# Kernel optimization log

Hardware: AMD Instinct MI355X
Metric: run time of the kernel (lower is better)

The kernel has to match this reference:

```python
import jax, jax.numpy as jnp
import numpy as np

NUM_TAGS = 5

def setup_inputs() -> dict:
    key = jax.random.key(0)
    ks = jax.random.split(key, 8)
    B, N, K, Q = 2, 5, 5, 4
    Ls, Lq, D = 128, 128, 768
    inp = {
        'support_token_embedding': jax.random.normal(ks[0], (B * N * K, Ls, D), jnp.float32),
        'query_token_embedding': jax.random.normal(ks[1], (B * N * Q, Lq, D), jnp.float32),
        'support_mask': jnp.ones((B * N * K, Ls), jnp.float32),
        'query_mask': jnp.ones((B * N * Q, Lq), jnp.float32),
        'support_entity_label': jax.random.normal(ks[2], (B * N * K, Ls, NUM_TAGS), jnp.float32),
        'proj_w': jax.random.normal(ks[3], (D, 4 * D), jnp.float32) * 0.02,
        'proj_b': jnp.zeros((D,), jnp.float32),
        'rel_w1': jax.random.normal(ks[4], (D, 4 * D), jnp.float32) * 0.02,
        'rel_b1': jnp.zeros((D,), jnp.float32),
        'rel_w2': jax.random.normal(ks[5], (1, D), jnp.float32) * 0.02,
        'rel_b2': jnp.zeros((1,), jnp.float32),
        'B': B, 'N': N, 'K': K, 'Q': Q,
    }
    return inp

def _fuse(m1, m2):
    return jnp.concatenate([m1, m2, jnp.abs(m1 - m2), m1 * m2], axis=-1)

def reference(support_token_embedding, query_token_embedding, support_mask, query_mask,
              support_entity_label, proj_w, proj_b, rel_w1, rel_b1, rel_w2, rel_b2,
              B, N, K, Q):
    D = support_token_embedding.shape[-1]
    Lq = query_token_embedding.shape[1]

    # ---- cal_bio: per-(sample,shot) tag prototypes, vectorized ----
    labels = jnp.argmax(support_entity_label, axis=-1)                 # [BNK, Ls]
    onehot = jax.nn.one_hot(labels, NUM_TAGS, dtype=jnp.float32)       # [BNK, Ls, T]
    # tag 0 ('O') is additionally gated by the support mask
    masks = jnp.concatenate([onehot[:, :, :1] * support_mask[:, :, None], onehot[:, :, 1:]], axis=2)
    sums = jnp.einsum('blt,bld->btd', masks, support_token_embedding)  # [BNK, T, D]
    cnt = jnp.sum(masks, axis=1)[:, :, None]                           # [BNK, T, 1]
    proto = jnp.where(cnt > 0, sums / jnp.maximum(cnt, 1.0), 0.0)      # [BNK, T, D]
    proto = proto.reshape(B * N, K, NUM_TAGS, D).mean(axis=1)          # mean over K shots
    proto = proto.reshape(B, N, NUM_TAGS, D)                           # support_BIO

    # ---- expand to all (query, class) pairs: batch = B*N*Q*N ----
    BQ = B * N * Q * N
    support = jnp.broadcast_to(proto[:, None], (B, N * Q, N, NUM_TAGS, D)).reshape(BQ, NUM_TAGS, D)
    query = jnp.broadcast_to(query_token_embedding.reshape(B, N * Q, 1, Lq, D),
                             (B, N * Q, N, Lq, D)).reshape(BQ, Lq, D)
    qmask = jnp.broadcast_to(query_mask.reshape(B, N * Q, 1, Lq),
                             (B, N * Q, N, Lq)).reshape(BQ, Lq, 1)
    smask = jnp.ones((BQ, NUM_TAGS, 1), jnp.float32)

    # ---- CoAttention with additive mask bias + post-softmax mask multiply ----
    att = jnp.einsum('bsd,bqd->bsq', support, query) + smask * jnp.swapaxes(qmask, 1, 2) * 100.0
    support_ = jnp.einsum('bsq,bqd->bsd', jax.nn.softmax(att, axis=2), query) * smask
    query_ = jnp.einsum('bqs,bsd->bqd', jax.nn.softmax(jnp.swapaxes(att, 1, 2), axis=2), support) * qmask

    # ---- fuse + proj + relu ----
    es = jax.nn.relu(_fuse(support, support_) @ proj_w.T + proj_b)     # [BQ, T, D]
    eq = jax.nn.relu(_fuse(query, query_) @ proj_w.T + proj_b)        # [BQ, Lq, D]

    # ---- local aggregation: masked max + mean pooling ----
    eq_agg = jnp.concatenate([jnp.max(eq, axis=1), jnp.sum(eq, axis=1) / jnp.sum(qmask, axis=1)], axis=1)
    es_agg = jnp.concatenate([jnp.max(es, axis=1), jnp.sum(es, axis=1) / jnp.sum(smask, axis=1)], axis=1)

    # ---- relation MLP ----
    cat_seq = jnp.concatenate([eq_agg, es_agg], axis=1)                # [BQ, 4D]
    h = jax.nn.relu(cat_seq @ rel_w1.T + rel_b1)
    logits = h @ rel_w2.T + rel_b2                                     # [BQ, 1]
    return logits.reshape(B * N * Q, N)
```

## Files before the change

### kernel.cpp

```cpp
#include <hip/hip_runtime.h>

typedef unsigned short u16;
typedef __attribute__((ext_vector_type(8))) short short8;
typedef __attribute__((ext_vector_type(4))) float f32x4;

#define B_   2
#define N_   5
#define K_   5
#define Q_   4
#define T_   5
#define D_   768
#define L_   128
#define BN_  (B_*N_)
#define BNK_ (B_*N_*K_)
#define BQ_  (B_*N_*Q_*N_)
#define K4_  (4*D_)
#define KFQ  1536
#define AROWS 144

#define QEMB_N  (40*128*768)
#define PROJW_N (768*3072)

__device__ __forceinline__ float bf2f(u16 u) {
    return __uint_as_float(((unsigned)u) << 16);
}
__device__ __forceinline__ u16 f2bf(float f) {
    unsigned u = __float_as_uint(f);
    return (u16)((u + 0x7fffu + ((u >> 16) & 1u)) >> 16);
}
__device__ __forceinline__ void gl_lds16(const u16* g, u16* l) {
    __builtin_amdgcn_global_load_lds(
        (const __attribute__((address_space(1))) unsigned int*)g,
        (__attribute__((address_space(3))) unsigned int*)l, 16, 0, 0);
}

__global__ void k_convert3(const float* __restrict__ q, const float* __restrict__ pw,
                           const float* __restrict__ rw, u16* __restrict__ qo,
                           u16* __restrict__ po, u16* __restrict__ ro) {
    const long n1 = QEMB_N / 4, n2 = PROJW_N / 4;
    const long total = n1 + 2 * n2;
    for (long i = (long)blockIdx.x * 256 + threadIdx.x; i < total; i += (long)gridDim.x * 256) {
        const float* src; u16* dst; long k;
        if (i < n1)            { src = q;  dst = qo; k = i; }
        else if (i < n1 + n2)  { src = pw; dst = po; k = i - n1; }
        else                   { src = rw; dst = ro; k = i - n1 - n2; }
        float4 v = ((const float4*)src)[k];
        u16 o[4] = {f2bf(v.x), f2bf(v.y), f2bf(v.z), f2bf(v.w)};
        *(uint2*)(dst + k * 4) = *(const uint2*)o;
    }
}

__global__ void k_proto_shot(const float* __restrict__ label, const float* __restrict__ smask,
                             const float* __restrict__ semb, float* __restrict__ proto_shot) {
    int bnk = blockIdx.x;
    int s = blockIdx.y;
    __shared__ int   s_tag[L_];
    __shared__ float s_w[L_];
    __shared__ float s_cnt[T_];
    int tid = threadIdx.x;
    if (tid < L_) {
        const float* lp = label + ((long)bnk * L_ + tid) * T_;
        float best = lp[0]; int bi = 0;
        #pragma unroll
        for (int t = 1; t < T_; ++t) { float v = lp[t]; if (v > best) { best = v; bi = t; } }
        s_tag[tid] = bi;
        s_w[tid]   = (bi == 0) ? smask[(long)bnk * L_ + tid] : 1.0f;
    }
    __syncthreads();
    if (tid < T_) {
        float c = 0.f;
        for (int l = 0; l < L_; ++l) if (s_tag[l] == tid) c += s_w[l];
        s_cnt[tid] = c;
    }
    __syncthreads();
    float acc[T_] = {};
    for (int l = 0; l < L_; ++l) {
        float w = s_w[l]; int tg = s_tag[l];
        float e = semb[((long)bnk * L_ + l) * D_ + tid + s * 256] * w;
        #pragma unroll
        for (int t = 0; t < T_; ++t) acc[t] += (tg == t) ? e : 0.0f;
    }
    int d = tid + s * 256;
    #pragma unroll
    for (int t = 0; t < T_; ++t) {
        float c = s_cnt[t];
        float v = (c > 0.f) ? acc[t] / fmaxf(c, 1.f) : 0.f;
        proto_shot[(bnk * T_ + t) * D_ + d] = v;
    }
}

__global__ void k_proto_mean(const float* __restrict__ proto_shot,
                             float* __restrict__ proto_f32, u16* __restrict__ proto_bf) {
    int idx = blockIdx.x * 256 + threadIdx.x;
    if (idx >= BN_ * T_ * D_) return;
    int bn = idx / (T_ * D_);
    int rem = idx - bn * (T_ * D_);
    float s = 0.f;
    #pragma unroll
    for (int k = 0; k < K_; ++k) s += proto_shot[(bn * K_ + k) * (T_ * D_) + rem];
    s *= (1.f / K_);
    proto_f32[idx] = s;
    proto_bf[idx]  = f2bf(s);
}

__global__ void k_attn(const float* __restrict__ qemb, const float* __restrict__ qmask_g,
                       const float* __restrict__ proto_f32,
                       u16* __restrict__ qf, u16* __restrict__ sup_ws,
                       float* __restrict__ p2m_ws, float* __restrict__ qssum_ws) {
    int x = blockIdx.x;
    int xcd = x & 7, slot = x >> 3;
    int g = (slot / 5) * 8 + xcd;
    int n2 = slot % 5;
    int bq = g * 5 + n2;
    int q_idx = g;
    int bn = (bq / (N_ * Q_ * N_)) * N_ + (bq % N_);
    __shared__ float s_proto[T_ * D_];
    __shared__ float s_att[T_][L_];
    __shared__ float s_ps[T_][L_];
    __shared__ float s_p2[L_][8];
    __shared__ float s_qm[L_];
    __shared__ float s_m2[L_][33];
    int tid = threadIdx.x;
    for (int i = tid; i < T_ * D_; i += 256) s_proto[i] = proto_f32[bn * T_ * D_ + i];
    if (tid < L_) s_qm[tid] = qmask_g[(long)q_idx * L_ + tid];
    __syncthreads();
    for (int p = tid; p < T_ * L_; p += 256) {
        int t = p >> 7, q = p & (L_ - 1);
        const float* pp = s_proto + t * D_;
        const float4* qp = (const float4*)(qemb + ((size_t)q_idx * L_ + q) * D_);
        float acc = 0.f;
        #pragma unroll 4
        for (int d = 0; d < D_ / 4; ++d) {
            float4 v = qp[d];
            acc += v.x * pp[4 * d] + v.y * pp[4 * d + 1] + v.z * pp[4 * d + 2] + v.w * pp[4 * d + 3];
        }
        s_att[t][q] = acc + 100.f * s_qm[q];
    }
    __syncthreads();
    if (tid < T_) {
        int t = tid; float m = -1e30f;
        for (int q = 0; q < L_; ++q) m = fmaxf(m, s_att[t][q]);
        float ss = 0.f;
        for (int q = 0; q < L_; ++q) { float e = __expf(s_att[t][q] - m); s_ps[t][q] = e; ss += e; }
        float inv = 1.f / ss;
        for (int q = 0; q < L_; ++q) s_ps[t][q] *= inv;
    } else if (tid >= 128) {
        int q = tid - 128; float m = -1e30f;
        float e[T_];
        #pragma unroll
        for (int t = 0; t < T_; ++t) m = fmaxf(m, s_att[t][q]);
        float ss = 0.f;
        #pragma unroll
        for (int t = 0; t < T_; ++t) { e[t] = __expf(s_att[t][q] - m); ss += e[t]; }
        float inv = s_qm[q] / ss;
        #pragma unroll
        for (int t = 0; t < T_; ++t) {
            s_p2[q][t] = e[t] * inv;
            p2m_ws[((size_t)bq * T_ + t) * L_ + q] = e[t] * inv;
        }
    } else if (tid == 5) {
        float s = 0.f;
        for (int q = 0; q < L_; ++q) s += s_qm[q];
        qssum_ws[bq] = s;
    }
    __syncthreads();
    u16* qfb = qf + (size_t)bq * AROWS * KFQ;
    {
        float acc[T_][3] = {};
        #pragma unroll 4
        for (int q = 0; q < L_; ++q) {
            const float* qp = qemb + ((size_t)q_idx * L_ + q) * D_;
            float qv[3];
            #pragma unroll
            for (int s = 0; s < 3; ++s) qv[s] = qp[tid + s * 256];
            #pragma unroll
            for (int t = 0; t < T_; ++t) {
                float p = s_ps[t][q];
                #pragma unroll
                for (int s = 0; s < 3; ++s) acc[t][s] += p * qv[s];
            }
        }
        #pragma unroll
        for (int t = 0; t < T_; ++t) {
            u16* er = qfb + (size_t)(128 + t) * KFQ;
            #pragma unroll
            for (int s = 0; s < 3; ++s) {
                int d = tid + s * 256;
                float p = s_proto[t * D_ + d];
                float sv = acc[t][s];
                sup_ws[((size_t)bq * T_ + t) * D_ + d] = f2bf(sv);
                er[d]       = f2bf(fabsf(p - sv));
                er[768 + d] = f2bf(p * sv);
            }
        }
    }
    {
        int row_b = tid & 127, half = tid >> 7;
        float pr[T_];
        #pragma unroll
        for (int t = 0; t < T_; ++t) pr[t] = s_p2[row_b][t];
        int d2 = tid & 31, r0 = tid >> 5;
        for (int slab = 0; slab < 24; ++slab) {
            #pragma unroll
            for (int j = 0; j < 16; ++j) {
                int col = half * 16 + j;
                int d = slab * 32 + col;
                float m2 = pr[0] * s_proto[d] + pr[1] * s_proto[D_ + d]
                         + pr[2] * s_proto[2 * D_ + d] + pr[3] * s_proto[3 * D_ + d]
                         + pr[4] * s_proto[4 * D_ + d];
                s_m2[row_b][col] = m2;
            }
            __syncthreads();
            #pragma unroll
            for (int k = 0; k < 16; ++k) {
                int row = r0 + k * 8;
                int dd = slab * 32 + d2;
                float m2 = s_m2[row][d2];
                float qv = qemb[((size_t)q_idx * L_ + row) * D_ + dd];
                u16* qr = qfb + (size_t)row * KFQ;
                qr[dd]        = f2bf(fabsf(qv - m2));
                qr[768 + dd]  = f2bf(qv * m2);
            }
            __syncthreads();
        }
    }
    {
        u16* pr2 = qfb + (size_t)133 * KFQ;
        short8 z = short8{0, 0, 0, 0, 0, 0, 0, 0};
        for (int i = tid; i < (11 * KFQ) / 8; i += 256) *(short8*)(pr2 + i * 8) = z;
    }
}

#define SWZ(g, r) (((g) << 4) + ((r) ^ ((g) << 2)))
__global__ __launch_bounds__(256) void k_gemm_g1(const u16* __restrict__ qemb_bf,
                                                 const u16* __restrict__ proto_bf,
                                                 const u16* __restrict__ projw_bf,
                                                 u16* __restrict__ g1) {
    int mbase = blockIdx.y * 128;
    int jbase = blockIdx.x * 128;
    __shared__ __align__(16) u16 sA[8 * 512];
    __shared__ __align__(16) u16 sB[8 * 512];
    int tid = threadIdx.x;
    int lane = tid & 63, w = tid >> 6, quad = lane >> 4, l16 = lane & 15;
    f32x4 zero = {0.f, 0.f, 0.f, 0.f};
    f32x4 acc[8][2];
    #pragma unroll
    for (int rt = 0; rt < 8; ++rt) { acc[rt][0] = zero; acc[rt][1] = zero; }

    for (int kt = 0; kt < 24; ++kt) {
        int k0 = kt * 32;
        __syncthreads();
        #pragma unroll
        for (int j = 0; j < 2; ++j) {
            int v = tid + j * 256, row = v >> 2, g = v & 3;
            *(uint4*)(sB + (((row >> 4) << 6) + SWZ(g, row & 15)) * 8) =
                *(const uint4*)(projw_bf + (size_t)(jbase + row) * K4_ + k0 + g * 8);
            int grow = mbase + row;
            uint4 av = uint4{0u, 0u, 0u, 0u};
            if (grow < 5120)      av = *(const uint4*)(qemb_bf + (size_t)grow * D_ + k0 + g * 8);
            else if (grow < 5170) av = *(const uint4*)(proto_bf + (size_t)(grow - 5120) * D_ + k0 + g * 8);
            *(uint4*)(sA + (((row >> 4) << 6) + SWZ(g, row & 15)) * 8) = av;
        }
        __syncthreads();
        short8 af[8], bfr[2];
        #pragma unroll
        for (int rt = 0; rt < 8; ++rt)
            af[rt] = *(const short8*)(sA + ((rt << 6) + SWZ(quad, l16)) * 8);
        #pragma unroll
        for (int jj = 0; jj < 2; ++jj)
            bfr[jj] = *(const short8*)(sB + (((w * 2 + jj) << 6) + SWZ(quad, l16)) * 8);
        #pragma unroll
        for (int rt = 0; rt < 8; ++rt)
            #pragma unroll
            for (int jj = 0; jj < 2; ++jj)
                acc[rt][jj] = __builtin_amdgcn_mfma_f32_16x16x32_bf16(af[rt], bfr[jj], acc[rt][jj], 0, 0, 0);
    }
    #pragma unroll
    for (int jj = 0; jj < 2; ++jj) {
        int col = jbase + (w * 2 + jj) * 16 + l16;
        #pragma unroll
        for (int rt = 0; rt < 8; ++rt)
            #pragma unroll
            for (int r = 0; r < 4; ++r) {
                int row = mbase + rt * 16 + quad * 4 + r;
                g1[(size_t)row * D_ + col] = f2bf(acc[rt][jj][r]);
            }
    }
}

__global__ __launch_bounds__(256) void k_gemm_w2(const u16* __restrict__ sup_ws,
                                                 const u16* __restrict__ proto_bf,
                                                 const u16* __restrict__ projw_bf,
                                                 u16* __restrict__ sw2, u16* __restrict__ pw2) {
    int mbase = blockIdx.y * 128;
    int jbase = blockIdx.x * 128;
    __shared__ __align__(16) u16 sA[8 * 512];
    __shared__ __align__(16) u16 sB[8 * 512];
    int tid = threadIdx.x;
    int lane = tid & 63, w = tid >> 6, quad = lane >> 4, l16 = lane & 15;
    f32x4 zero = {0.f, 0.f, 0.f, 0.f};
    f32x4 acc[8][2];
    #pragma unroll
    for (int rt = 0; rt < 8; ++rt) { acc[rt][0] = zero; acc[rt][1] = zero; }

    for (int kt = 0; kt < 24; ++kt) {
        int k0 = kt * 32;
        __syncthreads();
        #pragma unroll
        for (int j = 0; j < 2; ++j) {
            int v = tid + j * 256, row = v >> 2, g = v & 3;
            *(uint4*)(sB + (((row >> 4) << 6) + SWZ(g, row & 15)) * 8) =
                *(const uint4*)(projw_bf + (size_t)(jbase + row) * K4_ + 768 + k0 + g * 8);
            int grow = mbase + row;
            uint4 av = uint4{0u, 0u, 0u, 0u};
            if (grow < 1000)      av = *(const uint4*)(sup_ws + (size_t)grow * D_ + k0 + g * 8);
            else if (grow < 1050) av = *(const uint4*)(proto_bf + (size_t)(grow - 1000) * D_ + k0 + g * 8);
            *(uint4*)(sA + (((row >> 4) << 6) + SWZ(g, row & 15)) * 8) = av;
        }
        __syncthreads();
        short8 af[8], bfr[2];
        #pragma unroll
        for (int rt = 0; rt < 8; ++rt)
            af[rt] = *(const short8*)(sA + ((rt << 6) + SWZ(quad, l16)) * 8);
        #pragma unroll
        for (int jj = 0; jj < 2; ++jj)
            bfr[jj] = *(const short8*)(sB + (((w * 2 + jj) << 6) + SWZ(quad, l16)) * 8);
        #pragma unroll
        for (int rt = 0; rt < 8; ++rt)
            #pragma unroll
            for (int jj = 0; jj < 2; ++jj)
                acc[rt][jj] = __builtin_amdgcn_mfma_f32_16x16x32_bf16(af[rt], bfr[jj], acc[rt][jj], 0, 0, 0);
    }
    #pragma unroll
    for (int jj = 0; jj < 2; ++jj) {
        int col = jbase + (w * 2 + jj) * 16 + l16;
        #pragma unroll
        for (int rt = 0; rt < 8; ++rt)
            #pragma unroll
            for (int r = 0; r < 4; ++r) {
                int row = mbase + rt * 16 + quad * 4 + r;
                if (row < 1000)      sw2[(size_t)row * D_ + col] = f2bf(acc[rt][jj][r]);
                else if (row < 1050) pw2[(size_t)(row - 1000) * D_ + col] = f2bf(acc[rt][jj][r]);
            }
    }
}

__global__ __launch_bounds__(256, 3) void k_gemm_q(
        const u16* __restrict__ qf, const u16* __restrict__ projw_bf,
        const float* __restrict__ projb, const u16* __restrict__ g1,
        const u16* __restrict__ pw2, const u16* __restrict__ sw2,
        const float* __restrict__ p2m, const float* __restrict__ qssum_ws,
        u16* __restrict__ cat_ws) {
    int x = blockIdx.x;
    int xcd = x & 7, slot = x >> 3;
    int bq = (slot / 12) * 8 + xcd;
    int jbase = (slot % 12) * 64;
    int q_idx = bq / N_;
    int bn = (bq / (N_ * Q_ * N_)) * N_ + (bq % N_);
    __shared__ __align__(16) u16 sT[2][(AROWS + 64) * 32];
    __shared__ float s_p2mL[T_ * 128];
    __shared__ float s_pw2L[T_ * 64];
    int tid = threadIdx.x;
    int lane = tid & 63, w = tid >> 6, quad = lane >> 4, l16 = lane & 15;
    int srow = lane >> 2, sko = lane & 3;
    const u16* Ab = qf + ((size_t)bq * AROWS + srow) * KFQ + sko * 8;
    const u16* Bb = projw_bf + (size_t)(jbase + srow) * K4_ + 1536 + sko * 8;

    f32x4 zero = {0.f, 0.f, 0.f, 0.f};
    f32x4 acc[9];
    #pragma unroll
    for (int rt = 0; rt < 9; ++rt) acc[rt] = zero;

    auto issue = [&](int kt, int b) {
        int k0 = kt * 32;
        u16* base = sT[b];
        gl_lds16(Ab + (size_t)(w * 16) * KFQ + k0, base + (w * 16) * 32);
        gl_lds16(Ab + (size_t)(64 + w * 16) * KFQ + k0, base + (64 + w * 16) * 32);
        if (w == 0) gl_lds16(Ab + (size_t)128 * KFQ + k0, base + 128 * 32);
        gl_lds16(Bb + (size_t)(w * 16) * K4_ + k0, base + (AROWS + w * 16) * 32);
    };

    issue(0, 0);
    for (int kt = 0; kt < KFQ / 32; ++kt) {
        int cur = kt & 1;
        __syncthreads();
        if (kt + 1 < KFQ / 32) issue(kt + 1, 1 - cur);
        const u16* base = sT[cur];
        short8 af[9], bf1;
        #pragma unroll
        for (int rt = 0; rt < 9; ++rt)
            af[rt] = *(const short8*)(base + (rt * 16 + l16) * 32 + quad * 8);
        bf1 = *(const short8*)(base + (AROWS + w * 16 + l16) * 32 + quad * 8);
        #pragma unroll
        for (int rt = 0; rt < 9; ++rt)
            acc[rt] = __builtin_amdgcn_mfma_f32_16x16x32_bf16(af[rt], bf1, acc[rt], 0, 0, 0);
    }
    for (int i = tid; i < T_ * 128; i += 256) s_p2mL[i] = p2m[(size_t)bq * (T_ * 128) + i];
    for (int i = tid; i < T_ * 64; i += 256)
        s_pw2L[i] = bf2f(pw2[(size_t)(bn * T_ + (i >> 6)) * D_ + jbase + (i & 63)]);
    __syncthreads();
    float inv_qs = 1.f / qssum_ws[bq];
    {
        int c = w * 16 + l16;
        int col = jbase + c;
        float bias = projb[col];
        float qmax = 0.f, qsum = 0.f, smax = 0.f, ssum = 0.f;
        #pragma unroll
        for (int rt = 0; rt < 8; ++rt) {
            #pragma unroll
            for (int r = 0; r < 4; ++r) {
                int row = rt * 16 + quad * 4 + r;
                float g1v = bf2f(g1[(size_t)(q_idx * 128 + row) * D_ + col]);
                float mix = s_p2mL[row] * s_pw2L[c]
                          + s_p2mL[128 + row] * s_pw2L[64 + c]
                          + s_p2mL[256 + row] * s_pw2L[128 + c]
                          + s_p2mL[384 + row] * s_pw2L[192 + c]
                          + s_p2mL[512 + row] * s_pw2L[256 + c];
                float v = fmaxf(acc[rt][r] + g1v + mix + bias, 0.f);
                qmax = fmaxf(qmax, v); qsum += v;
            }
        }
        #pragma unroll
        for (int r = 0; r < 4; ++r) {
            int t = quad * 4 + r;
            if (t < T_) {
                float g1v = bf2f(g1[(size_t)(5120 + bn * T_ + t) * D_ + col]);
                float s2v = bf2f(sw2[(size_t)(bq * T_ + t) * D_ + col]);
                float v = fmaxf(acc[8][r] + g1v + s2v + bias, 0.f);
                smax = fmaxf(smax, v); ssum += v;
            }
        }
        qmax = fmaxf(qmax, __shfl_xor(qmax, 16, 64)); qmax = fmaxf(qmax, __shfl_xor(qmax, 32, 64));
        qsum += __shfl_xor(qsum, 16, 64);             qsum += __shfl_xor(qsum, 32, 64);
        smax = fmaxf(smax, __shfl_xor(smax, 16, 64)); smax = fmaxf(smax, __shfl_xor(smax, 32, 64));
        ssum += __shfl_xor(ssum, 16, 64);             ssum += __shfl_xor(ssum, 32, 64);
        if (quad == 0) {
            u16* cp = cat_ws + (size_t)bq * K4_;
            cp[col]           = f2bf(qmax);
            cp[D_ + col]      = f2bf(qsum * inv_qs);
            cp[2 * D_ + col]  = f2bf(smax);
            cp[3 * D_ + col]  = f2bf(ssum * 0.2f);
        }
    }
}

#define AST  40
__global__ __launch_bounds__(256) void k_relmlp(const u16* __restrict__ cat_ws,
                                                const u16* __restrict__ w1,
                                                float* __restrict__ part) {
    int mbase = blockIdx.y * 64;
    int jbase = blockIdx.x * 128;
    int ks = blockIdx.z;
    __shared__ __align__(16) u16 sA[64 * AST];
    __shared__ __align__(16) u16 sB[128 * AST];
    int tid = threadIdx.x;
    int lane = tid & 63, w = tid >> 6, quad = lane >> 4, l16 = lane & 15;
    f32x4 zero = {0.f, 0.f, 0.f, 0.f};
    f32x4 acc[4][2];
    #pragma unroll
    for (int rt = 0; rt < 4; ++rt) { acc[rt][0] = zero; acc[rt][1] = zero; }

    for (int kt = ks * 12; kt < ks * 12 + 12; ++kt) {
        int k0 = kt * 32;
        __syncthreads();
        {
            int row = tid >> 2, ko = (tid & 3) * 8;
            int grow = mbase + row;
            short8 val = short8{0, 0, 0, 0, 0, 0, 0, 0};
            if (grow < BQ_) val = *(const short8*)(cat_ws + (size_t)grow * K4_ + k0 + ko);
            *(short8*)(sA + row * AST + ko) = val;
        }
        for (int u = tid; u < 512; u += 256) {
            int row = u >> 2, ko = (u & 3) * 8;
            *(short8*)(sB + row * AST + ko) =
                *(const short8*)(w1 + (size_t)(jbase + row) * K4_ + k0 + ko);
        }
        __syncthreads();
        short8 af[4], bfr[2];
        #pragma unroll
        for (int rt = 0; rt < 4; ++rt)
            af[rt] = *(const short8*)(sA + (rt * 16 + l16) * AST + quad * 8);
        #pragma unroll
        for (int jj = 0; jj < 2; ++jj)
            bfr[jj] = *(const short8*)(sB + ((2 * w + jj) * 16 + l16) * AST + quad * 8);
        #pragma unroll
        for (int rt = 0; rt < 4; ++rt)
            #pragma unroll
            for (int jj = 0; jj < 2; ++jj)
                acc[rt][jj] = __builtin_amdgcn_mfma_f32_16x16x32_bf16(af[rt], bfr[jj], acc[rt][jj], 0, 0, 0);
    }
    #pragma unroll
    for (int jj = 0; jj < 2; ++jj) {
        int col = jbase + (2 * w + jj) * 16 + l16;
        #pragma unroll
        for (int rt = 0; rt < 4; ++rt) {
            #pragma unroll
            for (int r = 0; r < 4; ++r) {
                int grow = mbase + rt * 16 + quad * 4 + r;
                if (grow < BQ_)
                    part[((size_t)ks * BQ_ + grow) * D_ + col] = acc[rt][jj][r];
            }
        }
    }
}

__global__ void k_rel_fin(const float* __restrict__ part, const float* __restrict__ b1,
                          const float* __restrict__ w2, const float* __restrict__ b2,
                          float* __restrict__ out) {
    int bq = blockIdx.x, tid = threadIdx.x;
    float a = 0.f;
    #pragma unroll
    for (int s = 0; s < 3; ++s) {
        int col = tid + s * 256;
        float sum = 0.f;
        #pragma unroll
        for (int ks = 0; ks < 8; ++ks) sum += part[((size_t)ks * BQ_ + bq) * D_ + col];
        float h = fmaxf(sum + b1[col], 0.f);
        a += h * w2[col];
    }
    __shared__ float red[256];
    red[tid] = a; __syncthreads();
    for (int off = 128; off >= 1; off >>= 1) {
        if (tid < off) red[tid] += red[tid + off];
        __syncthreads();
    }
    if (tid == 0) out[bq] = red[0] + b2[0];
}

extern "C" void kernel_launch(void* const* d_in, const int* in_sizes, int n_in,
                              void* d_out, int out_size, void* d_ws, size_t ws_size,
                              hipStream_t stream) {
    (void)in_sizes; (void)n_in; (void)out_size; (void)ws_size;
    const float* semb  = (const float*)d_in[0];
    const float* qemb  = (const float*)d_in[1];
    const float* smask = (const float*)d_in[2];
    const float* qmask = (const float*)d_in[3];
    const float* label = (const float*)d_in[4];
    const float* projw = (const float*)d_in[5];
    const float* projb = (const float*)d_in[6];
    const float* relw1 = (const float*)d_in[7];
    const float* relb1 = (const float*)d_in[8];
    const float* relw2 = (const float*)d_in[9];
    const float* relb2 = (const float*)d_in[10];

    char* ws = (char*)d_ws;
    u16*   qemb_bf   = (u16*)  (ws + 0);
    u16*   projw_bf  = (u16*)  (ws + 7864320);
    u16*   relw1_bf  = (u16*)  (ws + 12582912);
    float* proto_shot= (float*)(ws + 17301504);
    float* proto_f32 = (float*)(ws + 18069504);
    u16*   proto_bf  = (u16*)  (ws + 18223104);
    float* qssum     = (float*)(ws + 18299904);
    u16*   sup_ws    = (u16*)  (ws + 18300800);
    float* p2m_ws    = (float*)(ws + 19836800);
    u16*   pw2_ws    = (u16*)  (ws + 20348800);
    u16*   sw2_ws    = (u16*)  (ws + 20425600);
    u16*   cat_ws    = (u16*)  (ws + 21961600);
    u16*   g1_ws     = (u16*)  (ws + 23190400);
    float* part_ws   = (float*)(ws + 31251328);
    u16*   qf_ws     = (u16*)  (ws + 36166528);

    k_convert3<<<2048, 256, 0, stream>>>(qemb, projw, relw1, qemb_bf, projw_bf, relw1_bf);
    k_proto_shot<<<dim3(BNK_, 3), 256, 0, stream>>>(label, smask, semb, proto_shot);
    k_proto_mean<<<150, 256, 0, stream>>>(proto_shot, proto_f32, proto_bf);
    k_attn<<<BQ_, 256, 0, stream>>>(qemb, qmask, proto_f32, qf_ws, sup_ws, p2m_ws, qssum);
    k_gemm_g1<<<dim3(6, 41), 256, 0, stream>>>(qemb_bf, proto_bf, projw_bf, g1_ws);
    k_gemm_w2<<<dim3(6, 9), 256, 0, stream>>>(sup_ws, proto_bf, projw_bf, sw2_ws, pw2_ws);
    k_gemm_q<<<2400, 256, 0, stream>>>(qf_ws, projw_bf, projb, g1_ws, pw2_ws, sw2_ws,
                                       p2m_ws, qssum, cat_ws);
    k_relmlp<<<dim3(6, 4, 8), 256, 0, stream>>>(cat_ws, relw1_bf, part_ws);
    k_rel_fin<<<BQ_, 256, 0, stream>>>(part_ws, relb1, relw2, relb2, (float*)d_out);
}
```

Measured before the change: 535.9 us.

## Widen k_gemm_q column tile to 128 and regroup blocks by query

Each k_gemm_q block now computes 128 output columns instead of 64, with each wave holding two B fragments and reusing every A fragment load across two MFMAs. This halves the grid and halves how many times the 144-row query-feature A tile is streamed from memory. The block-to-(bq, column) mapping is also reordered so consecutive slots on an XCD share the same bq group. In exchange the block needs more accumulator registers and more LDS, which may reduce occupancy under launch_bounds(256,3).

Measured after the change: 583.9 us. 1.09x slower.

```diff
diff --git a/kernel.cpp b/kernel.cpp
--- a/kernel.cpp
+++ b/kernel.cpp
@@ -353,13 +353,15 @@
         u16* __restrict__ cat_ws) {
     int x = blockIdx.x;
     int xcd = x & 7, slot = x >> 3;
-    int bq = (slot / 12) * 8 + xcd;
-    int jbase = (slot % 12) * 64;
+    int i = slot / 6, jslot = slot % 6;
+    int g = (i / 5) * 8 + xcd;
+    int bq = g * 5 + (i % 5);
+    int jbase = jslot * 128;
     int q_idx = bq / N_;
     int bn = (bq / (N_ * Q_ * N_)) * N_ + (bq % N_);
-    __shared__ __align__(16) u16 sT[2][(AROWS + 64) * 32];
+    __shared__ __align__(16) u16 sT[2][(AROWS + 128) * 32];
     __shared__ float s_p2mL[T_ * 128];
-    __shared__ float s_pw2L[T_ * 64];
+    __shared__ float s_pw2L[T_ * 128];
     int tid = threadIdx.x;
     int lane = tid & 63, w = tid >> 6, quad = lane >> 4, l16 = lane & 15;
     int srow = lane >> 2, sko = lane & 3;
@@ -367,9 +369,9 @@
     const u16* Bb = projw_bf + (size_t)(jbase + srow) * K4_ + 1536 + sko * 8;
 
     f32x4 zero = {0.f, 0.f, 0.f, 0.f};
-    f32x4 acc[9];
-    #pragma unroll
-    for (int rt = 0; rt < 9; ++rt) acc[rt] = zero;
+    f32x4 acc[9][2];
+    #pragma unroll
+    for (int rt = 0; rt < 9; ++rt) { acc[rt][0] = zero; acc[rt][1] = zero; }
 
     auto issue = [&](int kt, int b) {
         int k0 = kt * 32;
@@ -378,6 +380,7 @@
         gl_lds16(Ab + (size_t)(64 + w * 16) * KFQ + k0, base + (64 + w * 16) * 32);
         if (w == 0) gl_lds16(Ab + (size_t)128 * KFQ + k0, base + 128 * 32);
         gl_lds16(Bb + (size_t)(w * 16) * K4_ + k0, base + (AROWS + w * 16) * 32);
+        gl_lds16(Bb + (size_t)(64 + w * 16) * K4_ + k0, base + (AROWS + 64 + w * 16) * 32);
     };
 
     issue(0, 0);
@@ -386,23 +389,27 @@
         __syncthreads();
         if (kt + 1 < KFQ / 32) issue(kt + 1, 1 - cur);
         const u16* base = sT[cur];
-        short8 af[9], bf1;
-        #pragma unroll
-        for (int rt = 0; rt < 9; ++rt)
-            af[rt] = *(const short8*)(base + (rt * 16 + l16) * 32 + quad * 8);
-        bf1 = *(const short8*)(base + (AROWS + w * 16 + l16) * 32 + quad * 8);
-        #pragma unroll
-        for (int rt = 0; rt < 9; ++rt)
-            acc[rt] = __builtin_amdgcn_mfma_f32_16x16x32_bf16(af[rt], bf1, acc[rt], 0, 0, 0);
-    }
-    for (int i = tid; i < T_ * 128; i += 256) s_p2mL[i] = p2m[(size_t)bq * (T_ * 128) + i];
-    for (int i = tid; i < T_ * 64; i += 256)
-        s_pw2L[i] = bf2f(pw2[(size_t)(bn * T_ + (i >> 6)) * D_ + jbase + (i & 63)]);
+        short8 bfr[2];
+        #pragma unroll
+        for (int jj = 0; jj < 2; ++jj)
+            bfr[jj] = *(const short8*)(base + (AROWS + (w * 2 + jj) * 16 + l16) * 32 + quad * 8);
+        #pragma unroll
+        for (int rt = 0; rt < 9; ++rt) {
+            short8 a = *(const short8*)(base + (rt * 16 + l16) * 32 + quad * 8);
+            acc[rt][0] = __builtin_amdgcn_mfma_f32_16x16x32_bf16(a, bfr[0], acc[rt][0], 0, 0, 0);
+            acc[rt][1] = __builtin_amdgcn_mfma_f32_16x16x32_bf16(a, bfr[1], acc[rt][1], 0, 0, 0);
+        }
+    }
+    for (int i2 = tid; i2 < T_ * 128; i2 += 256) {
+        s_p2mL[i2] = p2m[(size_t)bq * (T_ * 128) + i2];
+        s_pw2L[i2] = bf2f(pw2[(size_t)(bn * T_ + (i2 >> 7)) * D_ + jbase + (i2 & 127)]);
+    }
     __syncthreads();
     float inv_qs = 1.f / qssum_ws[bq];
-    {
-        int c = w * 16 + l16;
-        int col = jbase + c;
+    #pragma unroll
+    for (int jj = 0; jj < 2; ++jj) {
+        int col = jbase + (w * 2 + jj) * 16 + l16;
+        int cj = (w * 2 + jj) * 16 + l16;
         float bias = projb[col];
         float qmax = 0.f, qsum = 0.f, smax = 0.f, ssum = 0.f;
         #pragma unroll
@@ -411,12 +418,12 @@
             for (int r = 0; r < 4; ++r) {
                 int row = rt * 16 + quad * 4 + r;
                 float g1v = bf2f(g1[(size_t)(q_idx * 128 + row) * D_ + col]);
-                float mix = s_p2mL[row] * s_pw2L[c]
-                          + s_p2mL[128 + row] * s_pw2L[64 + c]
-                          + s_p2mL[256 + row] * s_pw2L[128 + c]
-                          + s_p2mL[384 + row] * s_pw2L[192 + c]
-                          + s_p2mL[512 + row] * s_pw2L[256 + c];
-                float v = fmaxf(acc[rt][r] + g1v + mix + bias, 0.f);
+                float mix = s_p2mL[row] * s_pw2L[cj]
+                          + s_p2mL[128 + row] * s_pw2L[128 + cj]
+                          + s_p2mL[256 + row] * s_pw2L[256 + cj]
+                          + s_p2mL[384 + row] * s_pw2L[384 + cj]
+                          + s_p2mL[512 + row] * s_pw2L[512 + cj];
+                float v = fmaxf(acc[rt][jj][r] + g1v + mix + bias, 0.f);
                 qmax = fmaxf(qmax, v); qsum += v;
             }
         }
@@ -426,7 +433,7 @@
             if (t < T_) {
                 float g1v = bf2f(g1[(size_t)(5120 + bn * T_ + t) * D_ + col]);
                 float s2v = bf2f(sw2[(size_t)(bq * T_ + t) * D_ + col]);
-                float v = fmaxf(acc[8][r] + g1v + s2v + bias, 0.f);
+                float v = fmaxf(acc[8][jj][r] + g1v + s2v + bias, 0.f);
                 smax = fmaxf(smax, v); ssum += v;
             }
         }
@@ -566,7 +573,7 @@
     k_attn<<<BQ_, 256, 0, stream>>>(qemb, qmask, proto_f32, qf_ws, sup_ws, p2m_ws, qssum);
     k_gemm_g1<<<dim3(6, 41), 256, 0, stream>>>(qemb_bf, proto_bf, projw_bf, g1_ws);
     k_gemm_w2<<<dim3(6, 9), 256, 0, stream>>>(sup_ws, proto_bf, projw_bf, sw2_ws, pw2_ws);
-    k_gemm_q<<<2400, 256, 0, stream>>>(qf_ws, projw_bf, projb, g1_ws, pw2_ws, sw2_ws,
+    k_gemm_q<<<1200, 256, 0, stream>>>(qf_ws, projw_bf, projb, g1_ws, pw2_ws, sw2_ws,
                                        p2m_ws, qssum, cat_ws);
     k_relmlp<<<dim3(6, 4, 8), 256, 0, stream>>>(cat_ws, relw1_bf, part_ws);
     k_rel_fin<<<BQ_, 256, 0, stream>>>(part_ws, relb1, relw2, relb2, (float*)d_out);
```
